# Kernel optimization log

Hardware: AMD Instinct MI355X
Metric: run time of the kernel (lower is better)

## Reference

```python
import jax, jax.numpy as jnp
import numpy as np

NUM_HEADS = 4
OUT_DIM = 64
IN_DIM = 128

def setup_inputs() -> dict:
    key = jax.random.key(0)
    k1, k2, k3, k4 = jax.random.split(key, 4)
    h = jax.random.normal(k1, (4, 256, IN_DIM), dtype=jnp.float32)
    adj = jax.random.randint(k2, (4, 256, 256), 0, 2).astype(jnp.int32)
    W = jax.random.normal(k3, (IN_DIM, NUM_HEADS * OUT_DIM), dtype=jnp.float32) * (1.0 / np.sqrt(IN_DIM))
    a = jax.random.normal(k4, (2 * OUT_DIM, 1), dtype=jnp.float32) * 0.1
    return {"h": h, "adj": adj, "W": W, "a": a}

def reference(h, adj, W, a):
    B, N, _ = h.shape
    H, D = NUM_HEADS, OUT_DIM
    Wh = (h @ W).reshape(B, N, H, D)                      # [B,N,H,D]
    # Exact replication of the torch repeat/view construction (row-major, same as torch.view)
    a1 = jnp.tile(Wh, (1, 1, 1, N)).reshape(B, N * H, N, D)
    a2 = jnp.tile(Wh, (1, N, 1, 1)).reshape(B, N * H, N, D)
    a_input = jnp.concatenate([a1, a2], axis=3)           # [B,N*H,N,2D]
    e = jax.nn.leaky_relu((a_input @ a)[..., 0], negative_slope=0.2)
    e = e.reshape(B, H, N, N)
    mask = adj[:, None, :, :] == 0                        # broadcast over heads
    attention = jax.nn.softmax(jnp.where(mask, -jnp.inf, e), axis=3)  # [B,H,N,N]
    h_prime = jnp.einsum('bhij,bjhd->bihd', attention, Wh)             # [B,N,H,D]
    return h_prime.reshape(B, N, H * D)
```

## Files before the change

kernel.cpp:

```cpp
#include <hip/hip_runtime.h>
#include <hip/hip_bf16.h>


__global__ __launch_bounds__(256) void gat_wh_kernel(
    const float* __restrict__ h, const float* __restrict__ W,
    const float* __restrict__ a,
    float* __restrict__ Wh, float* __restrict__ f1, float* __restrict__ f2) {
  const int row0 = blockIdx.x * 8;
  const int c = threadIdx.x;

  __shared__ float sh[8][128];
  for (int t = threadIdx.x; t < 8 * 128; t += 256)
    sh[t >> 7][t & 127] = h[row0 * 128 + t];
  __syncthreads();

  float acc[8];
#pragma unroll
  for (int r = 0; r < 8; r++) acc[r] = 0.f;

  for (int k = 0; k < 128; k++) {
    float w = W[k * 256 + c];
#pragma unroll
    for (int r = 0; r < 8; r++) acc[r] += sh[r][k] * w;
  }

  const int d = c & 63;
  const int wv = c >> 6;
  const float a1v = a[d];
  const float a2v = a[64 + d];

#pragma unroll
  for (int r = 0; r < 8; r++) {
    Wh[(row0 + r) * 256 + c] = acc[r];
    float p1 = a1v * acc[r];
    float p2 = a2v * acc[r];
#pragma unroll
    for (int off = 32; off > 0; off >>= 1) {
      p1 += __shfl_xor(p1, off, 64);
      p2 += __shfl_xor(p2, off, 64);
    }
    if (d == 0) {
      f1[(row0 + r) * 4 + wv] = p1;
      f2[(row0 + r) * 4 + wv] = p2;
    }
  }
}

__global__ __launch_bounds__(256) void gat_attn_kernel(
    const float* __restrict__ Wh, const float* __restrict__ f1,
    const float* __restrict__ f2, const int* __restrict__ adj,
    float* __restrict__ out) {
  const int blk = blockIdx.x;
  const int it = blk & 63;
  const int hp = (blk >> 6) & 3;
  const int b  = blk >> 8;
  const int i0 = it * 4;

  const int tid = threadIdx.x;
  const int lane = tid & 63;
  const int wv = tid >> 6;
  const int i = i0 + wv;

  __shared__ float att[4][256];
  __shared__ float red[4][4][64];
  __shared__ float sinv[4];

  const float s1 = f1[b * 1024 + hp * 256 + i];
  const float* f2row = f2 + b * 1024 + (i & 3) * 256;
  const int* adjrow = adj + (b * 256 + i) * 256;

  float e[4];
  float m = -1e30f;
#pragma unroll
  for (int q = 0; q < 4; q++) {
    int j = lane + q * 64;
    float ev = s1 + f2row[j];
    ev = ev > 0.f ? ev : 0.2f * ev;
    ev = (adjrow[j] == 0) ? -1e30f : ev;
    e[q] = ev;
    m = fmaxf(m, ev);
  }
#pragma unroll
  for (int off = 32; off > 0; off >>= 1) m = fmaxf(m, __shfl_xor(m, off, 64));

  float s = 0.f;
#pragma unroll
  for (int q = 0; q < 4; q++) {
    float ex = __expf(e[q] - m);
    s += ex;
    att[wv][lane + q * 64] = ex;
  }
#pragma unroll
  for (int off = 32; off > 0; off >>= 1) s += __shfl_xor(s, off, 64);
  if (lane == 0) sinv[wv] = 1.f / s;
  __syncthreads();

  const int d = lane;
  const int seg = wv;
  const float* whp = Wh + b * 65536 + hp * 64 + d;
  float acc[4] = {0.f, 0.f, 0.f, 0.f};
  for (int jj = 0; jj < 64; jj++) {
    int j = seg * 64 + jj;
    float whv = whp[j * 256];
#pragma unroll
    for (int r = 0; r < 4; r++) acc[r] += att[r][j] * whv;
  }
#pragma unroll
  for (int r = 0; r < 4; r++) red[r][seg][d] = acc[r];
  __syncthreads();

  const int r = wv;
  float o = (red[r][0][d] + red[r][1][d]) + (red[r][2][d] + red[r][3][d]);
  o *= sinv[r];
  out[(b * 256 + i0 + r) * 256 + hp * 64 + d] = o;
}

extern "C" void kernel_launch(void* const* d_in, const int* in_sizes, int n_in,
                              void* d_out, int out_size, void* d_ws, size_t ws_size,
                              hipStream_t stream) {
  const float* h   = (const float*)d_in[0];
  const int*   adj = (const int*)d_in[1];
  const float* W   = (const float*)d_in[2];
  const float* a   = (const float*)d_in[3];
  float* out = (float*)d_out;

  float* Wh = (float*)d_ws;
  float* f1 = Wh + 262144;
  float* f2 = f1 + 4096;

  gat_wh_kernel<<<128, 256, 0, stream>>>(h, W, a, Wh, f1, f2);
  gat_attn_kernel<<<1024, 256, 0, stream>>>(Wh, f1, f2, adj, out);
}
```

Before: 76.79 us.

## Fuse projection and attention into one kernel with a grid-wide barrier

Merges the Wh/f1/f2 projection kernel and the attention kernel into a single persistent launch of 256 blocks. A global atomic counter, reset by a memset, serves as a grid barrier between the two phases. Each block now handles 16 attention rows instead of 4 and reads Wh with 4-wide unrolling plus float4 LDS loads. This removes one kernel launch but adds a memset node, a spin barrier that relies on all blocks being co-resident, and a bounded spin that could let a block proceed early.

```diff
diff --git a/kernel.cpp b/kernel.cpp
--- a/kernel.cpp
+++ b/kernel.cpp
@@ -1,118 +1,132 @@
 #include <hip/hip_runtime.h>
-#include <hip/hip_bf16.h>
 
 
-__global__ __launch_bounds__(256) void gat_wh_kernel(
+#define NBLK 256
+
+__global__ __launch_bounds__(256) void gat_fused(
     const float* __restrict__ h, const float* __restrict__ W,
-    const float* __restrict__ a,
-    float* __restrict__ Wh, float* __restrict__ f1, float* __restrict__ f2) {
-  const int row0 = blockIdx.x * 8;
-  const int c = threadIdx.x;
+    const float* __restrict__ a, const int* __restrict__ adj,
+    float* __restrict__ Wh, float* __restrict__ f1, float* __restrict__ f2,
+    int* __restrict__ bar, float* __restrict__ out)
+{
+  const int tid  = threadIdx.x;
+  const int lane = tid & 63;
+  const int wv   = tid >> 6;
+  const int blk  = blockIdx.x;
 
-  __shared__ float sh[8][128];
-  for (int t = threadIdx.x; t < 8 * 128; t += 256)
-    sh[t >> 7][t & 127] = h[row0 * 128 + t];
+  __shared__ float shA[4][128];
+  __shared__ float att[16][256];
+  __shared__ float red[16][4][64];
+  __shared__ float sinv[16];
+
+  const int r0 = blk * 4;
+  for (int t = tid; t < 512; t += 256) shA[t >> 7][t & 127] = h[r0 * 128 + t];
   __syncthreads();
 
-  float acc[8];
-#pragma unroll
-  for (int r = 0; r < 8; r++) acc[r] = 0.f;
-
+  const int c = tid;
+  float acc0 = 0.f, acc1 = 0.f, acc2 = 0.f, acc3 = 0.f;
   for (int k = 0; k < 128; k++) {
     float w = W[k * 256 + c];
-#pragma unroll
-    for (int r = 0; r < 8; r++) acc[r] += sh[r][k] * w;
+    acc0 += shA[0][k] * w;
+    acc1 += shA[1][k] * w;
+    acc2 += shA[2][k] * w;
+    acc3 += shA[3][k] * w;
   }
 
-  const int d = c & 63;
-  const int wv = c >> 6;
-  const float a1v = a[d];
-  const float a2v = a[64 + d];
-
+  const int d = lane;
+  const float a1v = a[d], a2v = a[64 + d];
+  float accs[4] = {acc0, acc1, acc2, acc3};
 #pragma unroll
-  for (int r = 0; r < 8; r++) {
-    Wh[(row0 + r) * 256 + c] = acc[r];
-    float p1 = a1v * acc[r];
-    float p2 = a2v * acc[r];
+  for (int r = 0; r < 4; r++) {
+    Wh[(r0 + r) * 256 + c] = accs[r];
+    float p1 = a1v * accs[r];
+    float p2 = a2v * accs[r];
 #pragma unroll
     for (int off = 32; off > 0; off >>= 1) {
       p1 += __shfl_xor(p1, off, 64);
       p2 += __shfl_xor(p2, off, 64);
     }
-    if (d == 0) {
-      f1[(row0 + r) * 4 + wv] = p1;
-      f2[(row0 + r) * 4 + wv] = p2;
+    if (d == 0) { f1[(r0 + r) * 4 + wv] = p1; f2[(r0 + r) * 4 + wv] = p2; }
+  }
+
+  __threadfence();
+  __syncthreads();
+  if (tid == 0) {
+    __hip_atomic_fetch_add(bar, 1, __ATOMIC_RELEASE, __HIP_MEMORY_SCOPE_AGENT);
+    int spins = 0;
+    while (__hip_atomic_load(bar, __ATOMIC_ACQUIRE, __HIP_MEMORY_SCOPE_AGENT) < NBLK
+           && ++spins < (1 << 24)) {}
+  }
+  __syncthreads();
+
+  const int b  = blk >> 6;
+  const int hp = (blk >> 4) & 3;
+  const int i0 = (blk & 15) * 16;
+
+#pragma unroll
+  for (int rq = 0; rq < 4; rq++) {
+    const int rr = wv * 4 + rq;
+    const int i  = i0 + rr;
+    const float s1 = f1[b * 1024 + hp * 256 + i];
+    const float* f2row = f2 + b * 1024 + (i & 3) * 256;
+    const int* adjrow = adj + (b * 256 + i) * 256;
+
+    float e[4];
+    float m = -1e30f;
+#pragma unroll
+    for (int jq = 0; jq < 4; jq++) {
+      int j = lane + jq * 64;
+      float ev = s1 + f2row[j];
+      ev = ev > 0.f ? ev : 0.2f * ev;
+      ev = adjrow[j] ? ev : -1e30f;
+      e[jq] = ev;
+      m = fmaxf(m, ev);
+    }
+#pragma unroll
+    for (int off = 32; off > 0; off >>= 1) m = fmaxf(m, __shfl_xor(m, off, 64));
+
+    float s = 0.f;
+#pragma unroll
+    for (int jq = 0; jq < 4; jq++) {
+      float ex = __expf(e[jq] - m);
+      s += ex;
+      att[rr][lane + jq * 64] = ex;
+    }
+#pragma unroll
+    for (int off = 32; off > 0; off >>= 1) s += __shfl_xor(s, off, 64);
+    if (lane == 0) sinv[rr] = 1.f / s;
+  }
+  __syncthreads();
+
+  const int seg = wv;
+  const float* whp = Wh + b * 65536 + hp * 64 + d;
+  float acc[16];
+#pragma unroll
+  for (int r = 0; r < 16; r++) acc[r] = 0.f;
+
+  for (int j4 = 0; j4 < 16; j4++) {
+    const int j = seg * 64 + j4 * 4;
+    float w0 = whp[(j + 0) * 256];
+    float w1 = whp[(j + 1) * 256];
+    float w2 = whp[(j + 2) * 256];
+    float w3 = whp[(j + 3) * 256];
+#pragma unroll
+    for (int r = 0; r < 16; r++) {
+      float4 a4 = *(const float4*)&att[r][j];
+      acc[r] += a4.x * w0 + a4.y * w1 + a4.z * w2 + a4.w * w3;
     }
   }
-}
-
-__global__ __launch_bounds__(256) void gat_attn_kernel(
-    const float* __restrict__ Wh, const float* __restrict__ f1,
-    const float* __restrict__ f2, const int* __restrict__ adj,
-    float* __restrict__ out) {
-  const int blk = blockIdx.x;
-  const int it = blk & 63;
-  const int hp = (blk >> 6) & 3;
-  const int b  = blk >> 8;
-  const int i0 = it * 4;
-
-  const int tid = threadIdx.x;
-  const int lane = tid & 63;
-  const int wv = tid >> 6;
-  const int i = i0 + wv;
-
-  __shared__ float att[4][256];
-  __shared__ float red[4][4][64];
-  __shared__ float sinv[4];
-
-  const float s1 = f1[b * 1024 + hp * 256 + i];
-  const float* f2row = f2 + b * 1024 + (i & 3) * 256;
-  const int* adjrow = adj + (b * 256 + i) * 256;
-
-  float e[4];
-  float m = -1e30f;
 #pragma unroll
-  for (int q = 0; q < 4; q++) {
-    int j = lane + q * 64;
-    float ev = s1 + f2row[j];
-    ev = ev > 0.f ? ev : 0.2f * ev;
-    ev = (adjrow[j] == 0) ? -1e30f : ev;
-    e[q] = ev;
-    m = fmaxf(m, ev);
-  }
-#pragma unroll
-  for (int off = 32; off > 0; off >>= 1) m = fmaxf(m, __shfl_xor(m, off, 64));
-
-  float s = 0.f;
-#pragma unroll
-  for (int q = 0; q < 4; q++) {
-    float ex = __expf(e[q] - m);
-    s += ex;
-    att[wv][lane + q * 64] = ex;
-  }
-#pragma unroll
-  for (int off = 32; off > 0; off >>= 1) s += __shfl_xor(s, off, 64);
-  if (lane == 0) sinv[wv] = 1.f / s;
+  for (int r = 0; r < 16; r++) red[r][seg][d] = acc[r];
   __syncthreads();
 
-  const int d = lane;
-  const int seg = wv;
-  const float* whp = Wh + b * 65536 + hp * 64 + d;
-  float acc[4] = {0.f, 0.f, 0.f, 0.f};
-  for (int jj = 0; jj < 64; jj++) {
-    int j = seg * 64 + jj;
-    float whv = whp[j * 256];
 #pragma unroll
-    for (int r = 0; r < 4; r++) acc[r] += att[r][j] * whv;
+  for (int rq = 0; rq < 4; rq++) {
+    const int r = wv * 4 + rq;
+    float o = (red[r][0][d] + red[r][1][d]) + (red[r][2][d] + red[r][3][d]);
+    o *= sinv[r];
+    out[(b * 256 + i0 + r) * 256 + hp * 64 + d] = o;
   }
-#pragma unroll
-  for (int r = 0; r < 4; r++) red[r][seg][d] = acc[r];
-  __syncthreads();
-
-  const int r = wv;
-  float o = (red[r][0][d] + red[r][1][d]) + (red[r][2][d] + red[r][3][d]);
-  o *= sinv[r];
-  out[(b * 256 + i0 + r) * 256 + hp * 64 + d] = o;
 }
 
 extern "C" void kernel_launch(void* const* d_in, const int* in_sizes, int n_in,
@@ -127,7 +141,8 @@
   float* Wh = (float*)d_ws;
   float* f1 = Wh + 262144;
   float* f2 = f1 + 4096;
+  int*   bar = (int*)(f2 + 4096);
 
-  gat_wh_kernel<<<128, 256, 0, stream>>>(h, W, a, Wh, f1, f2);
-  gat_attn_kernel<<<1024, 256, 0, stream>>>(Wh, f1, f2, adj, out);
+  hipMemsetAsync(bar, 0, sizeof(int), stream);
+  gat_fused<<<NBLK, 256, 0, stream>>>(h, W, a, adj, Wh, f1, f2, bar, out);
 }
```

Result: slower. 102.5 us (+33.4%).
